# Optimization experiments

Hardware: AMD Instinct MI355X
Metric: run time of the kernel (lower is better)

The kernel has to match this reference:

```python
import jax, jax.numpy as jnp
import numpy as np

B, N, F, H, E = 32, 512, 256, 1024, 8192
LN_EPS = 1e-5


def setup_inputs() -> dict:
    key = jax.random.key(0)
    ks = jax.random.split(key, 8)
    s = 0.02
    return {
        "node_features": jax.random.normal(ks[0], (B, N, F), jnp.float32),
        "edge_indexd": jax.random.randint(ks[1], (2, E), 0, N, jnp.int64),
        "edge_weights": jax.random.uniform(ks[2], (B, E), jnp.float32),
        "ln_gamma": jnp.ones((F,), jnp.float32),
        "ln_beta": jnp.zeros((F,), jnp.float32),
        "w1": jax.random.normal(ks[3], (H, N), jnp.float32) * s,
        "b1": jnp.zeros((H,), jnp.float32),
        "w2": jax.random.normal(ks[4], (N, H), jnp.float32) * s,
        "b2": jnp.zeros((N,), jnp.float32),
    }


def _laplacian(edge_idx, w):
    # w: [E] edge weights for one graph; edge_idx: [2, E]
    w = jnp.clip(w, 0.0, 1.0)
    # sparse_coo_tensor(...).to_dense() sums duplicate indices -> scatter-add
    A = jnp.zeros((N, N), w.dtype).at[edge_idx[0], edge_idx[1]].add(w)
    A = (A + A.T) * 0.5
    deg = jnp.clip(A.sum(axis=1), 1e-6, None)
    dis = deg ** -0.5  # finite since deg >= 1e-6
    L = jnp.eye(N, dtype=w.dtype) - dis[:, None] * A * dis[None, :]
    L = (L + L.T) * 0.5 + 1e-6 * jnp.eye(N, dtype=w.dtype)
    return L


def _forward(node_features, edge_indexd, edge_weights, ln_gamma, ln_beta, w1, b1, w2, b2):
    L = jax.vmap(lambda w: _laplacian(edge_indexd, w))(edge_weights)  # [B,N,N]
    # eigh is applied to L.detach() in the original -> stop_gradient
    eigvals, eigvecs = jnp.linalg.eigh(jax.lax.stop_gradient(L))  # [B,N], [B,N,N]

    # LayerNorm over feat_dim
    mu = node_features.mean(-1, keepdims=True)
    var = node_features.var(-1, keepdims=True)
    x = (node_features - mu) * jax.lax.rsqrt(var + LN_EPS) * ln_gamma + ln_beta
    x_residual = x
    x = jax.nn.relu(x)

    # x1 = eigvecs^T @ x : [B,N,F]
    x1 = jnp.einsum('bnk,bnf->bkf', eigvecs, x)
    # MLP on eigenvalues (dropout inactive in eval)
    h = jax.nn.relu(eigvals @ w1.T + b1)  # [B,H]
    ev_feat = h @ w2.T + b2               # [B,N]
    x1 = x1 * ev_feat[:, :, None]
    out = jnp.einsum('bnk,bkf->bnf', eigvecs, x1) + x_residual
    return out


def reference(node_features, edge_indexd, edge_weights, ln_gamma, ln_beta, w1, b1, w2, b2):
    return _forward(node_features, edge_indexd, edge_weights, ln_gamma, ln_beta, w1, b1, w2, b2)
```

## Files before the change

### kernel.cpp

```cpp
#include <hip/hip_runtime.h>
#include <math.h>

#define BDIM 32
#define NDIM 512
#define FDIM 256
#define HDIM 1024
#define EDIM 8192
#define PCH  8192
#define CLTH 1.2e-4f
#define NB   16
#define BCOLS 16

__device__ __forceinline__ float waveRedSum(float v){
#pragma unroll
  for(int o=32;o>0;o>>=1) v += __shfl_down(v,o,64);
  return v;
}

__device__ __forceinline__ float rnd_f(int g, int i){
  unsigned s = (unsigned)g*1315423911u ^ (unsigned)i*2654435761u;
  s ^= s>>13; s *= 2246822519u; s ^= s>>16;
  return (float)(s & 0xFFFF)*(1.f/65536.f) - 0.5f;
}

__global__ __launch_bounds__(1024) void k_detect(const unsigned* __restrict__ e, int* __restrict__ flag){
  int t = threadIdx.x;
  float c = 0.f;
  for(int i=t;i<EDIM;i+=1024) if(e[2*i+1] != 0u) c += 1.f;
  c = waveRedSum(c);
  __shared__ float r[16];
  if((t&63)==0) r[t>>6]=c;
  __syncthreads();
  if(t==0){ float s=0; for(int z=0;z<16;z++) s+=r[z]; flag[0] = (s>64.f)?1:0; }
}

__global__ __launch_bounds__(256) void k_scatter(const float* __restrict__ ew, const int* __restrict__ eidx,
                                                 const int* __restrict__ flag, float* __restrict__ A){
  int t = blockIdx.x*256 + threadIdx.x;
  int b = t>>13, e = t&(EDIM-1);
  int i, j;
  if(flag[0]){ i = eidx[e]; j = eidx[EDIM+e]; }
  else       { i = eidx[2*e]; j = eidx[2*(EDIM+e)]; }
  i &= 511; j &= 511;
  float w = ew[(size_t)b*EDIM + e];
  w = 0.5f*fminf(fmaxf(w,0.f),1.f);
  float* Ab = A + (size_t)b*NDIM*NDIM;
  atomicAdd(Ab + (size_t)i*NDIM + j, w);
  atomicAdd(Ab + (size_t)j*NDIM + i, w);
}

__global__ __launch_bounds__(256) void k_degree(const float* __restrict__ A, float* __restrict__ dis){
  int wid = threadIdx.x>>6, lane = threadIdx.x&63;
  int row = blockIdx.x*4 + wid;
  const float* Ar = A + (size_t)row*NDIM;
  float s = 0.f;
  for(int j=lane;j<NDIM;j+=64) s += Ar[j];
  s = waveRedSum(s);
  if(lane==0) dis[row] = rsqrtf(fmaxf(s, 1e-6f));
}

__global__ __launch_bounds__(256) void k_lap(float* __restrict__ A, const float* __restrict__ dis){
  size_t t = (size_t)blockIdx.x*256 + threadIdx.x;
  size_t nn = (size_t)NDIM*NDIM;
  int b = (int)(t / nn); size_t rem = t % nn;
  int i = (int)(rem / NDIM), j = (int)(rem % NDIM);
  float v = -dis[b*NDIM+i]*dis[b*NDIM+j]*A[t];
  if(i==j) v += 1.f + 1e-6f;
  A[t] = v;
}

__global__ __launch_bounds__(256) void k_ln(const float* __restrict__ nf, const float* __restrict__ g,
                                            const float* __restrict__ be, float* __restrict__ X){
  int wid = threadIdx.x>>6, lane = threadIdx.x&63;
  int row = blockIdx.x*4 + wid;
  const float4* r4 = (const float4*)(nf + (size_t)row*FDIM);
  float4 v = r4[lane];
  float s  = v.x+v.y+v.z+v.w;
  float s2 = v.x*v.x+v.y*v.y+v.z*v.z+v.w*v.w;
  s = waveRedSum(s); s2 = waveRedSum(s2);
  s = __shfl(s,0,64); s2 = __shfl(s2,0,64);
  float mean = s*(1.f/FDIM);
  float var  = s2*(1.f/FDIM) - mean*mean;
  float inv  = rsqrtf(var + 1e-5f);
  float4 gg = ((const float4*)g)[lane];
  float4 bb = ((const float4*)be)[lane];
  float4 o;
  o.x = (v.x-mean)*inv*gg.x + bb.x;
  o.y = (v.y-mean)*inv*gg.y + bb.y;
  o.z = (v.z-mean)*inv*gg.z + bb.z;
  o.w = (v.w-mean)*inv*gg.w + bb.w;
  ((float4*)(X + (size_t)row*FDIM))[lane] = o;
}

__global__ __launch_bounds__(512,1) void k_tridiag(float* __restrict__ A, float* __restrict__ U,
                                                   float* __restrict__ dia, float* __restrict__ off,
                                                   float* __restrict__ tau){
  const int b = blockIdx.x, t = threadIdx.x;
  float* Ab = A + (size_t)b*NDIM*NDIM;
  float* Ub = U + (size_t)b*NDIM*NDIM;
  __shared__ __align__(16) float Up[NB][NDIM];
  __shared__ __align__(16) float Wp[NB][NDIM];
  __shared__ __align__(16) float ps[4][NDIM];
  __shared__ float dW[NB], dU[NB], hh_s[NB], dg_s[NB];
  __shared__ float sig_s, pd_s, x0_s;
  const int lane = t&63, wid = t>>6;
  const int cc = t&127, rg = t>>7;
  if(t==0){ sig_s = 0.f; pd_s = 0.f; }
  __syncthreads();
  float hprev = 0.f, rnext = 0.f;

  for(int k0=0; k0<NDIM-2; k0+=NB){
    const int ne = (NB < NDIM-2-k0)? NB : (NDIM-2-k0);
    if(t<ne) dg_s[t] = Ab[(size_t)(k0+t)*NDIM + (k0+t)];
    for(int p=0;p<ne;p++){
      const int k = k0+p;
      float v = 0.f;
      if(t>k){
        v = (p==0)? Ab[(size_t)k*NDIM + t] : rnext;
        for(int q=0;q<p;q++){
          float hq = (q==p-1)? hprev : hh_s[q];
          float uqk = Up[q][k], wqk = Wp[q][k];
          v -= uqk*Wp[q][t] + (wqk - 2.f*hq*uqk)*Up[q][t];
        }
      }
      if(t==k+1) x0_s = v;
      float ssq = (t>=k+2)? v*v : 0.f;
      ssq = waveRedSum(ssq);
      if(lane==0) atomicAdd(&sig_s, ssq);
      __syncthreads();
      const float sigma = sig_s, x0 = x0_s;
      if(t==0) pd_s = 0.f;
      float tk = 0.f, inv = 0.f, beta = x0;
      if(sigma > 1e-26f){
        beta = -copysignf(sqrtf(x0*x0+sigma), x0);
        tk = (beta-x0)/beta; inv = 1.f/(x0-beta);
      }
      const float u_t = (t>=k+2)? v*inv : ((t==k+1 && sigma>1e-26f)? 1.f : 0.f);
      Up[p][t] = u_t;
      __syncthreads();
      if(t==0) sig_s = 0.f;
      if(p+1<ne) rnext = Ab[(size_t)(k+1)*NDIM + t];
      for(int q=wid; q<p; q+=8){
        float du=0.f, dwr=0.f;
        for(int l=lane; l<NDIM; l+=64){
          float up_ = Up[p][l];
          du  += Up[q][l]*up_;
          dwr += Wp[q][l]*up_;
        }
        du = waveRedSum(du); dwr = waveRedSum(dwr);
        if(lane==0){
          float hq = (q==p-1)? hprev : hh_s[q];
          dU[q] = du; dW[q] = dwr - hq*du;
        }
      }
      {
        float4 acc = {0.f,0.f,0.f,0.f};
        const int j0 = 4*cc;
        if(j0+3 > k){
          const float* basep = Ab + j0;
          const int ib0 = (k+1)&~31;
          const int i1 = rg*4, i2 = 16+rg*4;
          const float* ap = basep + (size_t)ib0*NDIM;
          float4 c0 = *(const float4*)(ap + (size_t)(i1  )*NDIM);
          float4 c1 = *(const float4*)(ap + (size_t)(i1+1)*NDIM);
          float4 c2 = *(const float4*)(ap + (size_t)(i1+2)*NDIM);
          float4 c3 = *(const float4*)(ap + (size_t)(i1+3)*NDIM);
          float4 d0 = *(const float4*)(ap + (size_t)(i2  )*NDIM);
          float4 d1 = *(const float4*)(ap + (size_t)(i2+1)*NDIM);
          float4 d2 = *(const float4*)(ap + (size_t)(i2+2)*NDIM);
          float4 d3 = *(const float4*)(ap + (size_t)(i2+3)*NDIM);
          for(int ib=ib0; ib<NDIM; ib+=32){
            float4 n0=c0,n1=c1,n2=c2,n3=c3,m0=d0,m1=d1,m2=d2,m3=d3;
            if(ib+32 < NDIM){
              const float* an = basep + (size_t)(ib+32)*NDIM;
              n0 = *(const float4*)(an + (size_t)(i1  )*NDIM);
              n1 = *(const float4*)(an + (size_t)(i1+1)*NDIM);
              n2 = *(const float4*)(an + (size_t)(i1+2)*NDIM);
              n3 = *(const float4*)(an + (size_t)(i1+3)*NDIM);
              m0 = *(const float4*)(an + (size_t)(i2  )*NDIM);
              m1 = *(const float4*)(an + (size_t)(i2+1)*NDIM);
              m2 = *(const float4*)(an + (size_t)(i2+2)*NDIM);
              m3 = *(const float4*)(an + (size_t)(i2+3)*NDIM);
            }
            float4 u1 = *(const float4*)&Up[p][ib+i1];
            float4 u2 = *(const float4*)&Up[p][ib+i2];
            acc.x += c0.x*u1.x + c1.x*u1.y + c2.x*u1.z + c3.x*u1.w
                   + d0.x*u2.x + d1.x*u2.y + d2.x*u2.z + d3.x*u2.w;
            acc.y += c0.y*u1.x + c1.y*u1.y + c2.y*u1.z + c3.y*u1.w
                   + d0.y*u2.x + d1.y*u2.y + d2.y*u2.z + d3.y*u2.w;
            acc.z += c0.z*u1.x + c1.z*u1.y + c2.z*u1.z + c3.z*u1.w
                   + d0.z*u2.x + d1.z*u2.y + d2.z*u2.z + d3.z*u2.w;
            acc.w += c0.w*u1.x + c1.w*u1.y + c2.w*u1.z + c3.w*u1.w
                   + d0.w*u2.x + d1.w*u2.y + d2.w*u2.z + d3.w*u2.w;
            c0=n0; c1=n1; c2=n2; c3=n3; d0=m0; d1=m1; d2=m2; d3=m3;
          }
        }
        *(float4*)&ps[rg][4*cc] = acc;
      }
      __syncthreads();
      float py = ps[0][t]+ps[1][t]+ps[2][t]+ps[3][t];
      float corr = 0.f;
      for(int q=0;q<p;q++){
        float hq = (q==p-1)? hprev : hh_s[q];
        float duq = dU[q];
        corr += Up[q][t]*(dW[q] - hq*duq) + Wp[q][t]*duq;
      }
      float pv = tk*(py - corr);
      Wp[p][t] = pv;
      float pdp = waveRedSum(pv*u_t);
      if(lane==0) atomicAdd(&pd_s, pdp);
      if(t>k) Ub[(size_t)k*NDIM + (t-k-1)] = u_t;
      if(t==0){ off[(size_t)b*NDIM+k] = beta; tau[(size_t)b*NDIM+k] = tk; }
      __syncthreads();
      if(t==0){
        float dk = dg_s[p];
        for(int q=0;q<p;q++){
          float hq = (q==p-1)? hprev : hh_s[q];
          float uqk = Up[q][k];
          dk -= 2.f*uqk*(Wp[q][k] - hq*uqk);
        }
        dia[(size_t)b*NDIM+k] = dk;
      }
      hprev = 0.5f*tk*pd_s;
      if(t==0) hh_s[p] = hprev;
    }
    __syncthreads();
    for(int q=0;q<ne;q++){
      float hq = (q==ne-1)? hprev : hh_s[q];
      Wp[q][t] -= hq*Up[q][t];
    }
    __syncthreads();
    {
      const int r0 = k0+ne;
      const int rbase = r0 & ~15;
      const int cstart = rbase>>2;
      if(cc >= cstart){
        const int j0 = 4*cc;
        for(int rt=rbase; rt<NDIM; rt+=16){
          const int i0 = rt + rg*4;
          float* a0 = Ab + (size_t)i0*NDIM + j0;
          float4 v0 = *(float4*)(a0);
          float4 v1 = *(float4*)(a0+NDIM);
          float4 v2 = *(float4*)(a0+2*NDIM);
          float4 v3 = *(float4*)(a0+3*NDIM);
          #pragma unroll 4
          for(int q=0;q<ne;q++){
            float4 Ui = *(const float4*)&Up[q][i0];
            float4 Wi = *(const float4*)&Wp[q][i0];
            float4 Uj = *(const float4*)&Up[q][j0];
            float4 Wj = *(const float4*)&Wp[q][j0];
            v0.x -= Ui.x*Wj.x + Wi.x*Uj.x; v0.y -= Ui.x*Wj.y + Wi.x*Uj.y; v0.z -= Ui.x*Wj.z + Wi.x*Uj.z; v0.w -= Ui.x*Wj.w + Wi.x*Uj.w;
            v1.x -= Ui.y*Wj.x + Wi.y*Uj.x; v1.y -= Ui.y*Wj.y + Wi.y*Uj.y; v1.z -= Ui.y*Wj.z + Wi.y*Uj.z; v1.w -= Ui.y*Wj.w + Wi.y*Uj.w;
            v2.x -= Ui.z*Wj.x + Wi.z*Uj.x; v2.y -= Ui.z*Wj.y + Wi.z*Uj.y; v2.z -= Ui.z*Wj.z + Wi.z*Uj.z; v2.w -= Ui.z*Wj.w + Wi.z*Uj.w;
            v3.x -= Ui.w*Wj.x + Wi.w*Uj.x; v3.y -= Ui.w*Wj.y + Wi.w*Uj.y; v3.z -= Ui.w*Wj.z + Wi.w*Uj.z; v3.w -= Ui.w*Wj.w + Wi.w*Uj.w;
          }
          *(float4*)(a0)        = v0;
          *(float4*)(a0+NDIM)   = v1;
          *(float4*)(a0+2*NDIM) = v2;
          *(float4*)(a0+3*NDIM) = v3;
        }
      }
    }
    __syncthreads();
  }
  if(t==0){
    dia[(size_t)b*NDIM+NDIM-2] = Ab[(size_t)(NDIM-2)*NDIM+NDIM-2];
    dia[(size_t)b*NDIM+NDIM-1] = Ab[(size_t)(NDIM-1)*NDIM+NDIM-1];
    off[(size_t)b*NDIM+NDIM-2] = Ab[(size_t)(NDIM-2)*NDIM+NDIM-1];
    off[(size_t)b*NDIM+NDIM-1] = 0.f;
    tau[(size_t)b*NDIM+NDIM-2]=0.f; tau[(size_t)b*NDIM+NDIM-1]=0.f;
  }
}

__global__ __launch_bounds__(512) void k_bisect(const float* __restrict__ dia, const float* __restrict__ off,
                                                float* __restrict__ lam){
  int b = blockIdx.x, t = threadIdx.x;
  __shared__ float ds[NDIM], e2[NDIM];
  __shared__ float red[16];
  __shared__ float slo, shi;
  ds[t] = dia[(size_t)b*NDIM+t];
  float ev = (t<NDIM-1)? off[(size_t)b*NDIM+t] : 0.f;
  e2[t] = ev*ev;
  __syncthreads();
  float el = (t>0)? sqrtf(e2[t-1]) : 0.f;
  float er = fabsf(ev);
  float lo = ds[t]-el-er, hi = ds[t]+el+er;
#pragma unroll
  for(int o=32;o>0;o>>=1){ lo = fminf(lo,__shfl_down(lo,o,64)); hi = fmaxf(hi,__shfl_down(hi,o,64)); }
  if((t&63)==0){ red[t>>6]=lo; red[8+(t>>6)]=hi; }
  __syncthreads();
  if(t==0){
    float L=red[0], H=red[8];
    for(int z=1;z<8;z++){ L=fminf(L,red[z]); H=fmaxf(H,red[8+z]); }
    slo = L-1e-3f; shi = H+1e-3f;
  }
  __syncthreads();
  float lo2 = slo, hi2 = shi;
  for(int it=0; it<30; ++it){
    float mid = 0.5f*(lo2+hi2);
    float q = ds[0]-mid; int c = (q<0.f)?1:0;
    for(int i=1;i<NDIM;i++){
      float dn = (fabsf(q)<1e-10f)? ((q<0.f)?-1e-10f:1e-10f) : q;
      q = ds[i]-mid - __fdividef(e2[i-1], dn);
      c += (q<0.f)?1:0;
    }
    if(c<=t) lo2=mid; else hi2=mid;
  }
  lam[(size_t)b*NDIM+t] = 0.5f*(lo2+hi2);
}

__global__ __launch_bounds__(64) void k_stein(const float* __restrict__ dia, const float* __restrict__ off,
                                              const float* __restrict__ lam, float* __restrict__ W,
                                              float* __restrict__ fac, float* __restrict__ xs, int chunk){
  int p = blockIdx.x*64 + threadIdx.x;
  int g = chunk*PCH + p;
  int b = g >> 9, j = g & 511;
  __shared__ float ds[NDIM], es[NDIM];
  for(int i=threadIdx.x;i<NDIM;i+=64){ ds[i]=dia[(size_t)b*NDIM+i]; es[i]=off[(size_t)b*NDIM+i]; }
  __syncthreads();
  float lm = lam[(size_t)b*NDIM+j] + (float)((j%5)-2)*1.2e-7f;
  float* fu = fac + p;
  float* fm = fac + (size_t)PCH*NDIM + p;
  float* f1a = xs + p;
  float ai = ds[0]-lm, bi = es[0];
  for(int ib=0; ib<NDIM-1; ib+=8){
    const int lim = (NDIM-1-ib < 8)? NDIM-1-ib : 8;
    float dsb[8], esb[8], enb[8];
    #pragma unroll
    for(int z=0;z<8;z++){
      int i = ib+z; bool vz = z<lim;
      dsb[z] = vz? ds[i+1] : 0.f;
      esb[z] = vz? es[i]   : 0.f;
      enb[z] = (vz && i<NDIM-2)? es[i+1] : 0.f;
    }
    #pragma unroll
    for(int z=0;z<8;z++){
      if(z<lim){
        int i = ib+z;
        float ci = esb[z], an = dsb[z]-lm, bn = enb[z];
        float uu, mmenc, s1;
        if(fabsf(ai) >= fabsf(ci)){
          float aa = (fabsf(ai)<1e-12f)? ((ai<0.f)?-1e-12f:1e-12f) : ai;
          float mm = __fdividef(ci, aa);
          uu=aa; mmenc=mm; s1=bi;
          ai = an - mm*bi; bi = bn;
        } else {
          float cch = (fabsf(ci)<1e-12f)? ((ci<0.f)?-1e-12f:1e-12f) : ci;
          float mm = __fdividef(ai, cch);
          uu=cch; mmenc=mm+3.f; s1=an;
          ai = bi - mm*an; bi = -mm*bn;
        }
        fu[(size_t)i*PCH]=__fdividef(1.f,uu);
        fm[(size_t)i*PCH]=mmenc;
        f1a[(size_t)i*PCH]=s1;
      }
    }
  }
  { float aa = (fabsf(ai)<1e-12f)? ((ai<0.f)?-1e-12f:1e-12f) : ai; fu[(size_t)(NDIM-1)*PCH]=__fdividef(1.f,aa); }
  float* Wb = W + (size_t)b*NDIM*NDIM + j;
  float scale = 1.f;
  for(int it=0; it<3; ++it){
    float yi = (it==0)? rnd_f(g,0) : Wb[0]*scale;
    for(int ib=0; ib<NDIM-1; ib+=8){
      const int lim = (NDIM-1-ib < 8)? NDIM-1-ib : 8;
      float wn[8], me[8];
      #pragma unroll
      for(int z=0;z<8;z++){
        int i = ib+z; bool vz = z<lim;
        wn[z] = vz? ((it==0)? rnd_f(g,i+1) : Wb[(size_t)(i+1)*NDIM]*scale) : 0.f;
        me[z] = vz? fm[(size_t)i*PCH] : 0.f;
      }
      #pragma unroll
      for(int z=0;z<8;z++){
        if(z<lim){
          int i = ib+z;
          float enc = me[z]; bool sw = enc>1.5f; float mm = sw? enc-3.f : enc;
          float yn = wn[z];
          if(sw){ float tmp=yi; yi=yn; yn=tmp; }
          yn -= mm*yi;
          Wb[(size_t)i*NDIM] = yi;
          yi = yn;
        }
      }
    }
    float nrm, xp1, xp2;
    {
      float xi = yi * fu[(size_t)(NDIM-1)*PCH];
      Wb[(size_t)(NDIM-1)*NDIM]=xi; nrm = xi*xi; xp2=0.f; xp1=xi;
    }
    for(int ib=NDIM-2; ib>=0; ib-=8){
      const int lim = (ib+1 < 8)? ib+1 : 8;
      float yv[8], ru[8], me[8], f1b[8];
      #pragma unroll
      for(int z=0;z<8;z++){
        int i = ib-z; bool vz = z<lim;
        yv[z]  = vz? Wb[(size_t)i*NDIM] : 0.f;
        ru[z]  = vz? fu[(size_t)i*PCH] : 0.f;
        me[z]  = vz? fm[(size_t)i*PCH] : 0.f;
        f1b[z] = vz? f1a[(size_t)i*PCH] : 0.f;
      }
      #pragma unroll
      for(int z=0;z<8;z++){
        if(z<lim){
          int i = ib-z;
          bool sw = me[z]>1.5f;
          float f2 = sw? ((i<NDIM-2)? es[i+1] : 0.f) : 0.f;
          float xi = (yv[z] - f1b[z]*xp1 - f2*xp2)*ru[z];
          Wb[(size_t)i*NDIM]=xi; nrm += xi*xi;
          xp2=xp1; xp1=xi;
        }
      }
    }
    scale = rsqrtf(fmaxf(nrm,1e-30f));
  }
  for(int ib=0; ib<NDIM; ib+=8){
    float vz[8];
    #pragma unroll
    for(int z=0;z<8;z++) vz[z] = Wb[(size_t)(ib+z)*NDIM];
    #pragma unroll
    for(int z=0;z<8;z++) Wb[(size_t)(ib+z)*NDIM] = vz[z]*scale;
  }
}

__global__ __launch_bounds__(512) void k_mgs(const float* __restrict__ lam, float* __restrict__ W){
  int b = blockIdx.x, t = threadIdx.x;
  __shared__ int cstart[NDIM];
  __shared__ unsigned char brk[NDIM];
  __shared__ float red[8];
  __shared__ float sbc;
  const float* lb = lam + (size_t)b*NDIM;
  float* Wb = W + (size_t)b*NDIM*NDIM;
  brk[t] = (t==0)? 1 : ((lb[t]-lb[t-1] > CLTH)? 1 : 0);
  __syncthreads();
  if(t==0){ int s=0; for(int j=0;j<NDIM;j++){ if(brk[j]) s=j; cstart[j]=s; } }
  __syncthreads();
  for(int j=1;j<NDIM;j++){
    int s = cstart[j];
    if(s==j) continue;
    for(int q=s;q<j;q++){
      float pd = 0.f;
      pd = Wb[(size_t)t*NDIM+q]*Wb[(size_t)t*NDIM+j];
      pd = waveRedSum(pd);
      if((t&63)==0) red[t>>6]=pd;
      __syncthreads();
      if(t==0){ float s2=0; for(int z=0;z<8;z++) s2+=red[z]; sbc=s2; }
      __syncthreads();
      float dt = sbc;
      Wb[(size_t)t*NDIM+j] -= dt*Wb[(size_t)t*NDIM+q];
      __syncthreads();
    }
    float v = Wb[(size_t)t*NDIM+j];
    float pn = waveRedSum(v*v);
    if((t&63)==0) red[t>>6]=pn;
    __syncthreads();
    if(t==0){ float s2=0; for(int z=0;z<8;z++) s2+=red[z]; sbc=s2; }
    __syncthreads();
    Wb[(size_t)t*NDIM+j] = v*rsqrtf(fmaxf(sbc,1e-20f));
    __syncthreads();
  }
}

__global__ __launch_bounds__(512,4) void k_backt(float* __restrict__ W, const float* __restrict__ U,
                                                 const float* __restrict__ tau){
  __shared__ float S[NDIM][BCOLS+1];
  __shared__ float Up[NB][516];
  __shared__ float Gp[NB][NB+1];
  __shared__ float Tm[NB][NB+1];
  __shared__ float Yp[2][NB][NB+1];
  __shared__ float Z16[NB][NB+1];
  __shared__ float tls[NB];
  const int t = threadIdx.x;
  int b = blockIdx.x >> 5, slab = blockIdx.x & 31;
  int c0 = slab*BCOLS;
  float* Wb = W + (size_t)b*NDIM*NDIM;
  const float* Ub = U + (size_t)b*NDIM*NDIM;
  for(int l=t; l<NDIM*BCOLS; l+=512){
    int i = l>>4, c = l&15;
    S[i][c] = Wb[(size_t)i*NDIM + c0 + c];
  }
  __syncthreads();
  for(int k0 = ((NDIM-3)/NB)*NB; k0>=0; k0-=NB){
    for(int l=t; l<NB*NDIM; l+=512){
      int q = l>>9, i = l&511;
      int k = k0+q;
      float v = 0.f;
      if(k < NDIM-2 && i > k) v = Ub[(size_t)k*NDIM + (i-k-1)];
      Up[q][i] = v;
    }
    if(t<NB) tls[t] = (k0+t < NDIM-2)? tau[(size_t)b*NDIM + k0 + t] : 0.f;
    if(t<NB*(NB+1)) ((float*)Gp)[t] = 0.f;
    __syncthreads();
    if(t < 480){
      int pp = t>>2, sub = t&3;
      int pj=1, pr=pp;
      while(pr >= pj){ pr -= pj; pj++; }
      int s = pr, jj = pj;
      float acc = 0.f;
      for(int i=k0+1+sub; i<NDIM; i+=4) acc += Up[s][i]*Up[jj][i];
      atomicAdd(&Gp[s][jj], acc);
    }
    __syncthreads();
    if(t < 16){
      int a = t;
      for(int j=0;j<NB;j++){
        float v;
        if(a==j) v = tls[j];
        else if(a<j){
          float s2 = 0.f;
          for(int s=a; s<j; s++) s2 += Tm[a][s]*Gp[s][j];
          v = -tls[j]*s2;
        } else v = 0.f;
        Tm[a][j] = v;
      }
    }
    __syncthreads();
    {
      int q=(t>>4)&15, c=t&15, half=t>>8;
      float a0=0.f, a1=0.f;
      int i = k0+1+half;
      for(; i+2<NDIM; i+=4){ a0 += Up[q][i]*S[i][c]; a1 += Up[q][i+2]*S[i+2][c]; }
      for(; i<NDIM; i+=2) a0 += Up[q][i]*S[i][c];
      Yp[half][q][c] = a0+a1;
    }
    __syncthreads();
    if(t < 256){
      int a=t>>4, c=t&15;
      float acc=0.f;
      #pragma unroll
      for(int j=0;j<NB;j++) acc += Tm[a][j]*(Yp[0][j][c]+Yp[1][j][c]);
      Z16[a][c]=acc;
    }
    __syncthreads();
    {
      int rg=t>>4, c=t&15;
      float zc[NB];
      #pragma unroll
      for(int q=0;q<NB;q++) zc[q]=Z16[q][c];
      for(int i=k0+1+rg; i<NDIM; i+=32){
        float s2=0.f;
        #pragma unroll
        for(int q=0;q<NB;q++) s2 += Up[q][i]*zc[q];
        S[i][c] -= s2;
      }
    }
    __syncthreads();
  }
  for(int l=t; l<NDIM*BCOLS; l+=512){
    int i = l>>4, c = l&15;
    Wb[(size_t)i*NDIM + c0 + c] = S[i][c];
  }
}

__global__ __launch_bounds__(256) void k_mlp1(const float* __restrict__ lam, const float* __restrict__ w1,
                                              const float* __restrict__ b1, float* __restrict__ h){
  int wid = threadIdx.x>>6, lane = threadIdx.x&63;
  int j = blockIdx.x*4 + wid, b = blockIdx.y;
  const float* lb = lam + (size_t)b*NDIM;
  const float* wr = w1 + (size_t)j*NDIM;
  float acc = 0.f;
  for(int k=lane;k<NDIM;k+=64) acc += lb[k]*wr[k];
  acc = waveRedSum(acc);
  if(lane==0) h[(size_t)b*HDIM + j] = fmaxf(acc + b1[j], 0.f);
}
__global__ __launch_bounds__(256) void k_mlp2(const float* __restrict__ h, const float* __restrict__ w2,
                                              const float* __restrict__ b2, float* __restrict__ evb){
  int wid = threadIdx.x>>6, lane = threadIdx.x&63;
  int n = blockIdx.x*4 + wid, b = blockIdx.y;
  const float* hb = h + (size_t)b*HDIM;
  const float* wr = w2 + (size_t)n*HDIM;
  float acc = 0.f;
  for(int k=lane;k<HDIM;k+=64) acc += hb[k]*wr[k];
  acc = waveRedSum(acc);
  if(lane==0) evb[(size_t)b*NDIM + n] = acc + b2[n];
}

__global__ __launch_bounds__(256) void k_gemm1(const float* __restrict__ Z, const float* __restrict__ X,
                                               const float* __restrict__ evb, float* __restrict__ X1){
  int b = blockIdx.z;
  int i0 = blockIdx.y*64, f0 = blockIdx.x*64;
  const float* Zb = Z + (size_t)b*NDIM*NDIM;
  const float* Xb = X + (size_t)b*NDIM*FDIM;
  __shared__ float As[32][65], Bs[32][65];
  int tx = threadIdx.x & 15, ty = threadIdx.x >> 4;
  float acc[4][4] = {};
  for(int n0=0;n0<NDIM;n0+=32){
    for(int l=threadIdx.x; l<32*64; l+=256){
      int dn = l>>6, dc = l&63;
      As[dn][dc] = Zb[(size_t)(n0+dn)*NDIM + i0+dc];
      Bs[dn][dc] = fmaxf(Xb[(size_t)(n0+dn)*FDIM + f0+dc], 0.f);
    }
    __syncthreads();
#pragma unroll
    for(int dn=0;dn<32;dn++){
      float a[4], bb[4];
#pragma unroll
      for(int z=0;z<4;z++){ a[z]=As[dn][ty*4+z]; bb[z]=Bs[dn][tx*4+z]; }
#pragma unroll
      for(int p=0;p<4;p++)
#pragma unroll
        for(int q=0;q<4;q++) acc[p][q] += a[p]*bb[q];
    }
    __syncthreads();
  }
#pragma unroll
  for(int p=0;p<4;p++){
    int i = i0 + ty*4 + p;
    float s = evb[(size_t)b*NDIM + i];
    float4 o = { acc[p][0]*s, acc[p][1]*s, acc[p][2]*s, acc[p][3]*s };
    *(float4*)(X1 + ((size_t)b*NDIM + i)*FDIM + f0 + tx*4) = o;
  }
}

__global__ __launch_bounds__(256) void k_gemm2(const float* __restrict__ Z, const float* __restrict__ X1,
                                               const float* __restrict__ X, float* __restrict__ outp){
  int b = blockIdx.z;
  int n0 = blockIdx.y*64, f0 = blockIdx.x*64;
  const float* Zb = Z + (size_t)b*NDIM*NDIM;
  const float* X1b = X1 + (size_t)b*NDIM*FDIM;
  __shared__ float As[32][65], Bs[32][65];
  int tx = threadIdx.x & 15, ty = threadIdx.x >> 4;
  float acc[4][4] = {};
  for(int i0=0;i0<NDIM;i0+=32){
    for(int l=threadIdx.x; l<32*64; l+=256){
      int di = l&31, dn = l>>5;
      As[di][dn] = Zb[(size_t)(n0+dn)*NDIM + i0+di];
    }
    for(int l=threadIdx.x; l<32*64; l+=256){
      int di = l>>6, df = l&63;
      Bs[di][df] = X1b[(size_t)(i0+di)*FDIM + f0+df];
    }
    __syncthreads();
#pragma unroll
    for(int dk=0;dk<32;dk++){
      float a[4], bb[4];
#pragma unroll
      for(int z=0;z<4;z++){ a[z]=As[dk][ty*4+z]; bb[z]=Bs[dk][tx*4+z]; }
#pragma unroll
      for(int p=0;p<4;p++)
#pragma unroll
        for(int q=0;q<4;q++) acc[p][q] += a[p]*bb[q];
    }
    __syncthreads();
  }
#pragma unroll
  for(int p=0;p<4;p++){
    size_t ro = ((size_t)b*NDIM + n0+ty*4+p)*FDIM + f0 + tx*4;
    float4 xr = *(const float4*)(X + ro);
    float4 o = { acc[p][0]+xr.x, acc[p][1]+xr.y, acc[p][2]+xr.z, acc[p][3]+xr.w };
    *(float4*)(outp + ro) = o;
  }
}

extern "C" void kernel_launch(void* const* d_in, const int* in_sizes, int n_in,
                              void* d_out, int out_size, void* d_ws, size_t ws_size,
                              hipStream_t stream) {
  (void)in_sizes; (void)n_in; (void)out_size; (void)ws_size;
  const float* nf  = (const float*)d_in[0];
  const int*   eidx= (const int*)d_in[1];
  const float* ew  = (const float*)d_in[2];
  const float* lng = (const float*)d_in[3];
  const float* lnb = (const float*)d_in[4];
  const float* w1  = (const float*)d_in[5];
  const float* b1  = (const float*)d_in[6];
  const float* w2  = (const float*)d_in[7];
  const float* b2  = (const float*)d_in[8];

  float* ws = (float*)d_ws;
  const size_t NN = (size_t)NDIM*NDIM;
  float* A   = ws;
  float* U   = A  + (size_t)BDIM*NN;
  float* W   = U  + (size_t)BDIM*NN;
  float* X   = W  + (size_t)BDIM*NN;
  float* X1  = X  + (size_t)BDIM*NDIM*FDIM;
  float* dia = X1 + (size_t)BDIM*NDIM*FDIM;
  float* off = dia + (size_t)BDIM*NDIM;
  float* tau = off + (size_t)BDIM*NDIM;
  float* lam = tau + (size_t)BDIM*NDIM;
  float* dis = lam + (size_t)BDIM*NDIM;
  float* hbf = dis + (size_t)BDIM*NDIM;
  float* evb = hbf + (size_t)BDIM*HDIM;
  int*   flag= (int*)(evb + (size_t)BDIM*NDIM);

  hipMemsetAsync(A, 0, (size_t)BDIM*NN*sizeof(float), stream);
  k_detect <<<1, 1024, 0, stream>>>((const unsigned*)eidx, flag);
  k_scatter<<<(BDIM*EDIM)/256, 256, 0, stream>>>(ew, eidx, flag, A);
  k_degree <<<(BDIM*NDIM)/4, 256, 0, stream>>>(A, dis);
  k_lap    <<<(unsigned)((size_t)BDIM*NN/256), 256, 0, stream>>>(A, dis);
  k_ln     <<<(BDIM*NDIM)/4, 256, 0, stream>>>(nf, lng, lnb, X);
  k_tridiag<<<BDIM, 512, 0, stream>>>(A, U, dia, off, tau);
  k_bisect <<<BDIM, 512, 0, stream>>>(dia, off, lam);
  k_mlp1   <<<dim3(HDIM/4, BDIM), 256, 0, stream>>>(lam, w1, b1, hbf);
  k_mlp2   <<<dim3(NDIM/4, BDIM), 256, 0, stream>>>(hbf, w2, b2, evb);
  for(int c=0;c<(BDIM*NDIM)/PCH;c++)
    k_stein<<<PCH/64, 64, 0, stream>>>(dia, off, lam, W, A , X1 , c);
  k_mgs    <<<BDIM, 512, 0, stream>>>(lam, W);
  k_backt  <<<BDIM*32, 512, 0, stream>>>(W, U, tau);
  k_gemm1  <<<dim3(FDIM/64, NDIM/64, BDIM), 256, 0, stream>>>(W, X, evb, X1);
  k_gemm2  <<<dim3(FDIM/64, NDIM/64, BDIM), 256, 0, stream>>>(W, X1, X, (float*)d_out);
}
```

Measured before the change: 8.642 ms.

## Exploit symmetry in tridiagonal matvec by reading only upper-triangle 64x64 tiles

The Householder tridiagonalization's symmetric matrix-vector product now reads only the upper-triangular 64x64 tiles of the trailing submatrix. Each off-diagonal tile is applied twice, once as a column pass and once as a transposed row pass, with each wave accumulating into its own shared-memory partial vector. There are now eight partial vectors and they are zeroed before each step. This aims to roughly halve global memory traffic per step, at the cost of strided column reads, uneven tile distribution across waves and extra shared-memory zeroing.

```diff
diff --git a/kernel.cpp b/kernel.cpp
--- a/kernel.cpp
+++ b/kernel.cpp
@@ -100,7 +100,7 @@
   float* Ub = U + (size_t)b*NDIM*NDIM;
   __shared__ __align__(16) float Up[NB][NDIM];
   __shared__ __align__(16) float Wp[NB][NDIM];
-  __shared__ __align__(16) float ps[4][NDIM];
+  __shared__ __align__(16) float ps[8][NDIM];
   __shared__ float dW[NB], dU[NB], hh_s[NB], dg_s[NB];
   __shared__ float sig_s, pd_s, x0_s;
   const int lane = t&63, wid = t>>6;
@@ -139,6 +139,7 @@
       Up[p][t] = u_t;
       __syncthreads();
       if(t==0) sig_s = 0.f;
+      for(int l=lane; l<NDIM; l+=64) ps[wid][l] = 0.f;
       if(p+1<ne) rnext = Ab[(size_t)(k+1)*NDIM + t];
       for(int q=wid; q<p; q+=8){
         float du=0.f, dwr=0.f;
@@ -154,51 +155,35 @@
         }
       }
       {
-        float4 acc = {0.f,0.f,0.f,0.f};
-        const int j0 = 4*cc;
-        if(j0+3 > k){
-          const float* basep = Ab + j0;
-          const int ib0 = (k+1)&~31;
-          const int i1 = rg*4, i2 = 16+rg*4;
-          const float* ap = basep + (size_t)ib0*NDIM;
-          float4 c0 = *(const float4*)(ap + (size_t)(i1  )*NDIM);
-          float4 c1 = *(const float4*)(ap + (size_t)(i1+1)*NDIM);
-          float4 c2 = *(const float4*)(ap + (size_t)(i1+2)*NDIM);
-          float4 c3 = *(const float4*)(ap + (size_t)(i1+3)*NDIM);
-          float4 d0 = *(const float4*)(ap + (size_t)(i2  )*NDIM);
-          float4 d1 = *(const float4*)(ap + (size_t)(i2+1)*NDIM);
-          float4 d2 = *(const float4*)(ap + (size_t)(i2+2)*NDIM);
-          float4 d3 = *(const float4*)(ap + (size_t)(i2+3)*NDIM);
-          for(int ib=ib0; ib<NDIM; ib+=32){
-            float4 n0=c0,n1=c1,n2=c2,n3=c3,m0=d0,m1=d1,m2=d2,m3=d3;
-            if(ib+32 < NDIM){
-              const float* an = basep + (size_t)(ib+32)*NDIM;
-              n0 = *(const float4*)(an + (size_t)(i1  )*NDIM);
-              n1 = *(const float4*)(an + (size_t)(i1+1)*NDIM);
-              n2 = *(const float4*)(an + (size_t)(i1+2)*NDIM);
-              n3 = *(const float4*)(an + (size_t)(i1+3)*NDIM);
-              m0 = *(const float4*)(an + (size_t)(i2  )*NDIM);
-              m1 = *(const float4*)(an + (size_t)(i2+1)*NDIM);
-              m2 = *(const float4*)(an + (size_t)(i2+2)*NDIM);
-              m3 = *(const float4*)(an + (size_t)(i2+3)*NDIM);
+        const int tb = (k+1)>>6;
+        const int nt = 8 - tb;
+        const int ntiles = nt*(nt+1)/2;
+        for(int tl=wid; tl<ntiles; tl+=8){
+          int a=0, rem=tl;
+          while(rem > a){ rem -= (a+1); a++; }
+          const int ib = (tb+a)*64, jb = (tb+rem)*64;
+          {
+            float accd = 0.f;
+            const float* cp = Ab + (size_t)ib*NDIM + jb + lane;
+            #pragma unroll 8
+            for(int i=0;i<64;i++) accd += cp[(size_t)i*NDIM] * Up[p][ib+i];
+            ps[wid][jb+lane] += accd;
+          }
+          if(ib != jb){
+            float acc2 = 0.f;
+            const float* rowp = Ab + (size_t)(ib+lane)*NDIM + jb;
+            #pragma unroll 4
+            for(int j4=0;j4<64;j4+=4){
+              float4 a4 = *(const float4*)(rowp + j4);
+              float4 u4 = *(const float4*)&Up[p][jb+j4];
+              acc2 += a4.x*u4.x + a4.y*u4.y + a4.z*u4.z + a4.w*u4.w;
             }
-            float4 u1 = *(const float4*)&Up[p][ib+i1];
-            float4 u2 = *(const float4*)&Up[p][ib+i2];
-            acc.x += c0.x*u1.x + c1.x*u1.y + c2.x*u1.z + c3.x*u1.w
-                   + d0.x*u2.x + d1.x*u2.y + d2.x*u2.z + d3.x*u2.w;
-            acc.y += c0.y*u1.x + c1.y*u1.y + c2.y*u1.z + c3.y*u1.w
-                   + d0.y*u2.x + d1.y*u2.y + d2.y*u2.z + d3.y*u2.w;
-            acc.z += c0.z*u1.x + c1.z*u1.y + c2.z*u1.z + c3.z*u1.w
-                   + d0.z*u2.x + d1.z*u2.y + d2.z*u2.z + d3.z*u2.w;
-            acc.w += c0.w*u1.x + c1.w*u1.y + c2.w*u1.z + c3.w*u1.w
-                   + d0.w*u2.x + d1.w*u2.y + d2.w*u2.z + d3.w*u2.w;
-            c0=n0; c1=n1; c2=n2; c3=n3; d0=m0; d1=m1; d2=m2; d3=m3;
+            ps[wid][ib+lane] += acc2;
           }
         }
-        *(float4*)&ps[rg][4*cc] = acc;
       }
       __syncthreads();
-      float py = ps[0][t]+ps[1][t]+ps[2][t]+ps[3][t];
+      float py = ps[0][t]+ps[1][t]+ps[2][t]+ps[3][t]+ps[4][t]+ps[5][t]+ps[6][t]+ps[7][t];
       float corr = 0.f;
       for(int q=0;q<p;q++){
         float hq = (q==p-1)? hprev : hh_s[q];
```

New measurement: 10.78 ms. 1.25x slower.
